# Optimization experiments

Hardware: AMD Instinct MI355X
Metric: run time of the kernel (lower is better)

The kernel has to match this reference:

```python
import jax, jax.numpy as jnp
import numpy as np
from jax import lax

DN = ('NCHW', 'OIHW', 'NCHW')


def _conv(x, w, b, stride, dil):
    # spconv SparseConv2d on a dense field == VALID dense conv (zeros contribute zero)
    y = lax.conv_general_dilated(x, w, (stride, stride), 'VALID',
                                 rhs_dilation=(dil, dil), dimension_numbers=DN)
    return y + b[None, :, None, None]


def _inv_conv(y, w, b, stride, dil, k=3):
    # SparseInverseConv2d: exact transpose of the forward conv's spatial mapping.
    # On a dense field this is a transposed conv: lhs-dilate by stride, pad by
    # dil*(k-1) on each side, rhs-dilate by dil, with a spatially flipped kernel.
    pad = dil * (k - 1)
    wf = w[:, :, ::-1, ::-1]
    x = lax.conv_general_dilated(y, wf, (1, 1), [(pad, pad), (pad, pad)],
                                 lhs_dilation=(stride, stride),
                                 rhs_dilation=(dil, dil), dimension_numbers=DN)
    return x + b[None, :, None, None]


def setup_inputs() -> dict:
    key = jax.random.key(0)
    ks = jax.random.split(key, 9)
    B, Cin, H, W = 8, 3, 1021, 1021
    nc = 8
    s = 0.1
    return {
        'x':  jax.random.normal(ks[0], (B, Cin, H, W), jnp.float32),
        'w1': jax.random.normal(ks[1], (8, Cin, 3, 3), jnp.float32) * s,
        'b1': jax.random.normal(ks[2], (8,), jnp.float32) * s,
        'w2': jax.random.normal(ks[3], (16, 8, 3, 3), jnp.float32) * s,
        'b2': jax.random.normal(ks[4], (16,), jnp.float32) * s,
        'w3': jax.random.normal(ks[5], (8, 16, 3, 3), jnp.float32) * s,
        'b3': jax.random.normal(ks[6], (8,), jnp.float32) * s,
        'w4': jax.random.normal(ks[7], (nc, 8, 3, 3), jnp.float32) * s,
        'b4': jax.random.normal(ks[8], (nc,), jnp.float32) * s,
    }


def reference(x, w1, b1, w2, b2, w3, b3, w4, b4):
    h1 = jax.nn.relu(_conv(x, w1, b1, stride=2, dil=2))    # [B,8,509,509]
    h2 = jax.nn.relu(_conv(h1, w2, b2, stride=2, dil=2))   # [B,16,253,253]
    h3 = jax.nn.relu(_inv_conv(h2, w3, b3, stride=2, dil=2))  # [B,8,509,509]
    out = _inv_conv(h3, w4, b4, stride=2, dil=2)            # [B,nc,1021,1021]
    return out
```

## Files before the change

### kernel.cpp

```cpp
#include <hip/hip_runtime.h>

#define PLANE 1042441
#define S1 255
#define S2 253
#define S1S1 65025
#define S2S2 64009
#define NOUT 66716224


__global__ void k_setup(const float* __restrict__ w4, const float* __restrict__ b3_,
                        float* __restrict__ R, float* __restrict__ WT) {
  int t = threadIdx.x;
  if (t < 32) {
    int co = t >> 2, pc = t & 3;
    float s = 0.f;
    for (int ci = 0; ci < 8; ++ci) {
      float r3 = fmaxf(b3_[ci], 0.f);
      float wsum = 0.f;
      for (int jy = 0; jy < 3; ++jy)
        for (int jx = 0; jx < 3; ++jx) {
          bool cy = (pc & 2) ? (jy == 1) : (jy != 1);
          bool cx = (pc & 1) ? (jx == 1) : (jx != 1);
          if (!(cy && cx)) wsum += w4[(co * 8 + ci) * 9 + jy * 3 + jx];
        }
      s += r3 * wsum;
    }
    R[t] = s;
  }
  {
    int co = t >> 3, ci = t & 7;
    const float* w = w4 + (co * 8 + ci) * 9;
    float* d = WT + (co * 8 + ci) * 12;
    d[0] = w[0]; d[1] = w[2]; d[2] = w[6]; d[3] = w[8];
    d[4] = w[1]; d[5] = w[7]; d[6] = w[3]; d[7] = w[5];
    d[8] = w[4]; d[9] = 0.f; d[10] = 0.f; d[11] = 0.f;
  }
}

__global__ __launch_bounds__(256) void k_conv1(const float* __restrict__ x,
    const float* __restrict__ w1, const float* __restrict__ b1_, float* __restrict__ h1e) {
  int tx = threadIdx.x;
  int t0 = tx * 4;
  int m = blockIdx.y * 4 + threadIdx.y;
  if (m >= S1) return;
  int zb = blockIdx.z;
  int n = zb >> 1, cog = (zb & 1) * 4;

  float acc[4][4];
#pragma unroll
  for (int cc = 0; cc < 4; ++cc) {
    float b = b1_[cog + cc];
#pragma unroll
    for (int p = 0; p < 4; ++p) acc[cc][p] = b;
  }

  const float* xn = x + (size_t)n * 3 * PLANE;
  int b0 = 4 * t0;
  int o7 = b0 + 14 <= 1020 ? b0 + 14 : 1020;
  int o8 = b0 + 16 <= 1020 ? b0 + 16 : 1020;

#pragma unroll
  for (int ci = 0; ci < 3; ++ci) {
#pragma unroll
    for (int ky = 0; ky < 3; ++ky) {
      const float* xr = xn + ci * PLANE + (size_t)(4 * m + 2 * ky) * 1021u;
      float v[9];
      v[0] = xr[b0];      v[1] = xr[b0 + 2];  v[2] = xr[b0 + 4];
      v[3] = xr[b0 + 6];  v[4] = xr[b0 + 8];  v[5] = xr[b0 + 10];
      v[6] = xr[b0 + 12]; v[7] = xr[o7];      v[8] = xr[o8];
#pragma unroll
      for (int cc = 0; cc < 4; ++cc) {
        const float* w = w1 + (cog + cc) * 27 + ci * 9 + ky * 3;
        float w0 = w[0], w1v = w[1], w2v = w[2];
#pragma unroll
        for (int p = 0; p < 4; ++p)
          acc[cc][p] = fmaf(v[2 * p], w0, fmaf(v[2 * p + 1], w1v, fmaf(v[2 * p + 2], w2v, acc[cc][p])));
      }
    }
  }

#pragma unroll
  for (int cc = 0; cc < 4; ++cc) {
    float* op = h1e + ((size_t)(n * 8 + cog + cc) * S1 + m) * S1 + t0;
#pragma unroll
    for (int p = 0; p < 4; ++p)
      if (t0 + p < S1) op[p] = fmaxf(acc[cc][p], 0.f);
  }
}

__global__ __launch_bounds__(256) void k_conv2(const float* __restrict__ h1e,
    const float* __restrict__ w2, const float* __restrict__ b2_, float* __restrict__ h2) {
  int v0 = threadIdx.x * 4;
  int u = blockIdx.y * 4 + threadIdx.y;
  int zb = blockIdx.z;
  int n = zb >> 2, cog = (zb & 3) * 4;
  if (u >= S2) return;
  float acc[4][4];
#pragma unroll
  for (int cc = 0; cc < 4; ++cc) {
    float b = b2_[cog + cc];
#pragma unroll
    for (int p = 0; p < 4; ++p) acc[cc][p] = b;
  }
  const float* hn = h1e + (size_t)n * 8 * S1S1;
  for (int ci = 0; ci < 8; ++ci) {
    const float* hc = hn + ci * S1S1;
#pragma unroll
    for (int ky = 0; ky < 3; ++ky) {
      const float* hr = hc + (u + ky) * S1 + v0;
      float rr[6];
#pragma unroll
      for (int q = 0; q < 6; ++q) rr[q] = hr[q];
#pragma unroll
      for (int cc = 0; cc < 4; ++cc) {
        const float* w = w2 + (cog + cc) * 72 + ci * 9 + ky * 3;
        float w0 = w[0], w1 = w[1], w2v = w[2];
#pragma unroll
        for (int p = 0; p < 4; ++p)
          acc[cc][p] = fmaf(rr[p], w0, fmaf(rr[p + 1], w1, fmaf(rr[p + 2], w2v, acc[cc][p])));
      }
    }
  }
#pragma unroll
  for (int cc = 0; cc < 4; ++cc) {
    float* op = h2 + ((size_t)(n * 16 + cog + cc) * S2 + u) * S2 + v0;
#pragma unroll
    for (int p = 0; p < 4; ++p)
      if (v0 + p < S2) op[p] = fmaxf(acc[cc][p], 0.f);
  }
}

__global__ __launch_bounds__(256) void k_deconv3(const float* __restrict__ h2,
    const float* __restrict__ w3, const float* __restrict__ b3_, float* __restrict__ h3c) {
  int r0 = threadIdx.x * 4;
  int q = blockIdx.y * 4 + threadIdx.y;
  int zb = blockIdx.z;
  int n = zb >> 1, cog = (zb & 1) * 4;
  if (q >= S1) return;
  float acc[4][4];
#pragma unroll
  for (int cc = 0; cc < 4; ++cc) {
    float b = b3_[cog + cc];
#pragma unroll
    for (int p = 0; p < 4; ++p) acc[cc][p] = b;
  }
  const float* hn = h2 + (size_t)n * 16 * S2S2;
  bool inner = (r0 >= 4 && r0 <= 248);
  for (int ci = 0; ci < 16; ++ci) {
    const float* hc = hn + ci * S2S2;
#pragma unroll
    for (int jy = 0; jy < 3; ++jy) {
      int a = q - jy;
      if ((unsigned)a > 252u) continue;
      const float* hr = hc + a * S2 + (r0 - 2);
      float rr[6];
      if (inner) {
#pragma unroll
        for (int q2 = 0; q2 < 6; ++q2) rr[q2] = hr[q2];
      } else {
#pragma unroll
        for (int q2 = 0; q2 < 6; ++q2) {
          int col = r0 - 2 + q2;
          rr[q2] = ((unsigned)col <= 252u) ? hr[q2] : 0.f;
        }
      }
#pragma unroll
      for (int cc = 0; cc < 4; ++cc) {
        const float* w = w3 + ((cog + cc) * 16 + ci) * 9 + jy * 3;
        float w0 = w[0], w1 = w[1], w2v = w[2];
#pragma unroll
        for (int p = 0; p < 4; ++p)
          acc[cc][p] = fmaf(rr[p + 2], w0, fmaf(rr[p + 1], w1, fmaf(rr[p], w2v, acc[cc][p])));
      }
    }
  }
#pragma unroll
  for (int cc = 0; cc < 4; ++cc)
#pragma unroll
    for (int p = 0; p < 4; ++p)
      if (r0 + p < S1)
        h3c[((size_t)(n * 8 + cog + cc) * S1 + q) * S1 + r0 + p] = fmaxf(acc[cc][p], 0.f);
}

__device__ __forceinline__ float general_val(unsigned idx, const float* __restrict__ h3c,
    const float* __restrict__ w4, const float* __restrict__ b4_, const float* __restrict__ b3_) {
  unsigned z = idx / PLANE;
  unsigned rem = idx - z * PLANE;
  unsigned y = rem / 1021u;
  unsigned x = rem - y * 1021u;
  int co = z & 7;
  float acc = b4_[co];
  if ((y | x) & 1u) return acc;
  int py = y >> 1, px = x >> 1;
  const float* hn = h3c + (size_t)(z >> 3) * 8 * S1S1;
  const float* wp = w4 + co * 72;
  for (int ci = 0; ci < 8; ++ci) {
    float r3 = fmaxf(b3_[ci], 0.f);
    const float* hcc = hn + ci * S1S1;
#pragma unroll
    for (int jy = 0; jy < 3; ++jy) {
      int a = py - jy;
#pragma unroll
      for (int jx = 0; jx < 3; ++jx) {
        int b = px - jx;
        float h;
        if ((unsigned)a > 508u || (unsigned)b > 508u) h = 0.f;
        else if (((a | b) & 1) == 0) h = hcc[(a >> 1) * S1 + (b >> 1)];
        else h = r3;
        acc = fmaf(h, wp[ci * 9 + jy * 3 + jx], acc);
      }
    }
  }
  return acc;
}

__global__ __launch_bounds__(256) void k_out_rows(const float* __restrict__ h3c,
    const float* __restrict__ b4_, const float* __restrict__ R,
    const float* __restrict__ WT, float* __restrict__ out) {
  int t = threadIdx.x;
  int ye = blockIdx.x * 2;
  int z = blockIdx.y;
  int co = z & 7;
  float b4f = b4_[co];
  float* orow = out + (size_t)z * PLANE + (size_t)ye * 1021u;

  if (ye < 1020) {
    float* orow1 = orow + 1021;
    if (t < 255) *(float4*)(orow1 + 4 * t) = make_float4(b4f, b4f, b4f, b4f);
    else orow1[1020] = b4f;
  }

  if (ye < 4 || ye > 1016) return;
  if (t == 0 || t >= 254) return;
  unsigned py = (unsigned)ye >> 1;
  const float* hn = h3c + (size_t)(z >> 3) * 8 * S1S1;
  const float* wt = WT + co * 96;
  int col0 = t - 1;
  float vE = 0.f, vO = 0.f, rE, rO;
  if ((py & 1u) == 0) {
    unsigned i = py >> 1;
    const float* hp = hn + (i - 1) * S1 + col0;
#pragma unroll
    for (int ci = 0; ci < 8; ++ci) {
      const float* p = hp + ci * S1S1;
      float m00 = p[0], m01 = p[1], m10 = p[S1], m11 = p[S1 + 1];
      float4 A = *(const float4*)(wt + ci * 12);
      float4 B = *(const float4*)(wt + ci * 12 + 4);
      vE = fmaf(m11, A.x, fmaf(m10, A.y, fmaf(m01, A.z, fmaf(m00, A.w, vE))));
      vO = fmaf(m11, B.x, fmaf(m01, B.y, vO));
    }
    rE = b4f + R[co * 4 + 0] + vE;
    rO = b4f + R[co * 4 + 1] + vO;
  } else {
    unsigned a = py >> 1;
    const float* hp = hn + a * S1 + col0;
#pragma unroll
    for (int ci = 0; ci < 8; ++ci) {
      const float* p = hp + ci * S1S1;
      float n0 = p[0], n1 = p[1];
      float4 B = *(const float4*)(wt + ci * 12 + 4);
      float w11 = wt[ci * 12 + 8];
      vE = fmaf(n1, B.z, fmaf(n0, B.w, vE));
      vO = fmaf(n1, w11, vO);
    }
    rE = b4f + R[co * 4 + 2] + vE;
    rO = b4f + R[co * 4 + 3] + vO;
  }
  *(float4*)(orow + 4 * t) = make_float4(rE, b4f, rO, b4f);
}

__global__ __launch_bounds__(256) void k_out_border(const float* __restrict__ h3c,
    const float* __restrict__ w4, const float* __restrict__ b4_,
    const float* __restrict__ b3_, float* __restrict__ out) {
  int z = blockIdx.y;
  unsigned y, x;
  if (blockIdx.x < 18) {
    unsigned e = blockIdx.x * 256 + threadIdx.x;
    if (e >= 507u * 9u) return;
    unsigned r = e / 9u, c = e - r * 9u;
    y = 4u + 2u * r;
    x = (c < 4u) ? c : (1012u + c);
  } else {
    unsigned e2 = (blockIdx.x - 18) * 256 + threadIdx.x;
    if (e2 >= 4u * 1021u) return;
    unsigned rr = e2 / 1021u;
    y = (rr < 2u) ? 2u * rr : (1014u + 2u * rr);
    x = e2 - rr * 1021u;
  }
  unsigned idx = (unsigned)z * PLANE + y * 1021u + x;
  out[idx] = general_val(idx, h3c, w4, b4_, b3_);
}

extern "C" void kernel_launch(void* const* d_in, const int* in_sizes, int n_in,
                              void* d_out, int out_size, void* d_ws, size_t ws_size,
                              hipStream_t stream) {
  const float* x   = (const float*)d_in[0];
  const float* w1  = (const float*)d_in[1];
  const float* b1_ = (const float*)d_in[2];
  const float* w2  = (const float*)d_in[3];
  const float* b2_ = (const float*)d_in[4];
  const float* w3  = (const float*)d_in[5];
  const float* b3_ = (const float*)d_in[6];
  const float* w4  = (const float*)d_in[7];
  const float* b4_ = (const float*)d_in[8];
  float* out = (float*)d_out;

  float* h1e = (float*)d_ws;
  float* h2  = h1e + (size_t)8 * 8 * S1S1;
  float* h3c = h2 + (size_t)8 * 16 * S2S2;
  float* R   = h3c + (size_t)8 * 8 * S1S1;
  float* WT  = R + 32;

  k_setup<<<1, 64, 0, stream>>>(w4, b3_, R, WT);
  k_conv1<<<dim3(1, 64, 16), dim3(64, 4), 0, stream>>>(x, w1, b1_, h1e);
  k_conv2<<<dim3(1, 64, 32), dim3(64, 4), 0, stream>>>(h1e, w2, b2_, h2);
  k_deconv3<<<dim3(1, 64, 16), dim3(64, 4), 0, stream>>>(h2, w3, b3_, h3c);
  k_out_rows<<<dim3(511, 64), 256, 0, stream>>>(h3c, b4_, R, WT, out);
  k_out_border<<<dim3(34, 64), 256, 0, stream>>>(h3c, w4, b4_, b3_, out);
}
```

Baseline: 481.4 us.

## Compute eight output channels per thread in conv2/deconv3 and vectorize accesses

Each thread in k_conv2 and k_deconv3 now accumulates 8 output channels instead of 4. Every loaded input row is reused across twice as many channels, which halves the input reads and the grid size. Row loads and output stores now go through float4, even though the odd row strides (255, 253) make those addresses not 16-byte aligned. The trade-offs are higher register pressure and fewer blocks (512 for deconv3), which can lower occupancy and latency hiding.

```diff
diff --git a/kernel.cpp b/kernel.cpp
--- a/kernel.cpp
+++ b/kernel.cpp
@@ -93,11 +93,11 @@
   int v0 = threadIdx.x * 4;
   int u = blockIdx.y * 4 + threadIdx.y;
   int zb = blockIdx.z;
-  int n = zb >> 2, cog = (zb & 3) * 4;
+  int n = zb >> 1, cog = (zb & 1) * 8;
   if (u >= S2) return;
-  float acc[4][4];
-#pragma unroll
-  for (int cc = 0; cc < 4; ++cc) {
+  float acc[8][4];
+#pragma unroll
+  for (int cc = 0; cc < 8; ++cc) {
     float b = b2_[cog + cc];
 #pragma unroll
     for (int p = 0; p < 4; ++p) acc[cc][p] = b;
@@ -108,11 +108,10 @@
 #pragma unroll
     for (int ky = 0; ky < 3; ++ky) {
       const float* hr = hc + (u + ky) * S1 + v0;
-      float rr[6];
-#pragma unroll
-      for (int q = 0; q < 6; ++q) rr[q] = hr[q];
-#pragma unroll
-      for (int cc = 0; cc < 4; ++cc) {
+      float4 r4 = *(const float4*)hr;
+      float rr[6] = {r4.x, r4.y, r4.z, r4.w, hr[4], hr[5]};
+#pragma unroll
+      for (int cc = 0; cc < 8; ++cc) {
         const float* w = w2 + (cog + cc) * 72 + ci * 9 + ky * 3;
         float w0 = w[0], w1 = w[1], w2v = w[2];
 #pragma unroll
@@ -122,11 +121,16 @@
     }
   }
 #pragma unroll
-  for (int cc = 0; cc < 4; ++cc) {
+  for (int cc = 0; cc < 8; ++cc) {
     float* op = h2 + ((size_t)(n * 16 + cog + cc) * S2 + u) * S2 + v0;
-#pragma unroll
-    for (int p = 0; p < 4; ++p)
-      if (v0 + p < S2) op[p] = fmaxf(acc[cc][p], 0.f);
+    if (v0 + 3 < S2) {
+      *(float4*)op = make_float4(fmaxf(acc[cc][0], 0.f), fmaxf(acc[cc][1], 0.f),
+                                 fmaxf(acc[cc][2], 0.f), fmaxf(acc[cc][3], 0.f));
+    } else {
+#pragma unroll
+      for (int p = 0; p < 4; ++p)
+        if (v0 + p < S2) op[p] = fmaxf(acc[cc][p], 0.f);
+    }
   }
 }
 
@@ -134,13 +138,12 @@
     const float* __restrict__ w3, const float* __restrict__ b3_, float* __restrict__ h3c) {
   int r0 = threadIdx.x * 4;
   int q = blockIdx.y * 4 + threadIdx.y;
-  int zb = blockIdx.z;
-  int n = zb >> 1, cog = (zb & 1) * 4;
+  int n = blockIdx.z;
   if (q >= S1) return;
-  float acc[4][4];
-#pragma unroll
-  for (int cc = 0; cc < 4; ++cc) {
-    float b = b3_[cog + cc];
+  float acc[8][4];
+#pragma unroll
+  for (int cc = 0; cc < 8; ++cc) {
+    float b = b3_[cc];
 #pragma unroll
     for (int p = 0; p < 4; ++p) acc[cc][p] = b;
   }
@@ -155,8 +158,9 @@
       const float* hr = hc + a * S2 + (r0 - 2);
       float rr[6];
       if (inner) {
-#pragma unroll
-        for (int q2 = 0; q2 < 6; ++q2) rr[q2] = hr[q2];
+        float4 r4 = *(const float4*)hr;
+        rr[0] = r4.x; rr[1] = r4.y; rr[2] = r4.z; rr[3] = r4.w;
+        rr[4] = hr[4]; rr[5] = hr[5];
       } else {
 #pragma unroll
         for (int q2 = 0; q2 < 6; ++q2) {
@@ -165,8 +169,8 @@
         }
       }
 #pragma unroll
-      for (int cc = 0; cc < 4; ++cc) {
-        const float* w = w3 + ((cog + cc) * 16 + ci) * 9 + jy * 3;
+      for (int cc = 0; cc < 8; ++cc) {
+        const float* w = w3 + (cc * 16 + ci) * 9 + jy * 3;
         float w0 = w[0], w1 = w[1], w2v = w[2];
 #pragma unroll
         for (int p = 0; p < 4; ++p)
@@ -175,11 +179,17 @@
     }
   }
 #pragma unroll
-  for (int cc = 0; cc < 4; ++cc)
-#pragma unroll
-    for (int p = 0; p < 4; ++p)
-      if (r0 + p < S1)
-        h3c[((size_t)(n * 8 + cog + cc) * S1 + q) * S1 + r0 + p] = fmaxf(acc[cc][p], 0.f);
+  for (int cc = 0; cc < 8; ++cc) {
+    float* op = h3c + ((size_t)(n * 8 + cc) * S1 + q) * S1 + r0;
+    if (r0 + 3 < S1) {
+      *(float4*)op = make_float4(fmaxf(acc[cc][0], 0.f), fmaxf(acc[cc][1], 0.f),
+                                 fmaxf(acc[cc][2], 0.f), fmaxf(acc[cc][3], 0.f));
+    } else {
+#pragma unroll
+      for (int p = 0; p < 4; ++p)
+        if (r0 + p < S1) op[p] = fmaxf(acc[cc][p], 0.f);
+    }
+  }
 }
 
 __device__ __forceinline__ float general_val(unsigned idx, const float* __restrict__ h3c,
@@ -313,8 +323,8 @@
 
   k_setup<<<1, 64, 0, stream>>>(w4, b3_, R, WT);
   k_conv1<<<dim3(1, 64, 16), dim3(64, 4), 0, stream>>>(x, w1, b1_, h1e);
-  k_conv2<<<dim3(1, 64, 32), dim3(64, 4), 0, stream>>>(h1e, w2, b2_, h2);
-  k_deconv3<<<dim3(1, 64, 16), dim3(64, 4), 0, stream>>>(h2, w3, b3_, h3c);
+  k_conv2<<<dim3(1, 64, 16), dim3(64, 4), 0, stream>>>(h1e, w2, b2_, h2);
+  k_deconv3<<<dim3(1, 64, 8), dim3(64, 4), 0, stream>>>(h2, w3, b3_, h3c);
   k_out_rows<<<dim3(511, 64), 256, 0, stream>>>(h3c, b4_, R, WT, out);
   k_out_border<<<dim3(34, 64), 256, 0, stream>>>(h3c, w4, b4_, b3_, out);
 }
```

Result: no change. 472.3 us (-1.9%).
